# Performance work log

Measured on AMD Instinct MI355X. Metric: run time of the kernel, lower is better.

Reference implementation:

```python
import jax, jax.numpy as jnp
import numpy as np

B, C, N, K, COUT = 8, 128, 10000, 16, 256


def setup_inputs() -> dict:
    key = jax.random.key(0)
    ks = jax.random.split(key, 8)
    x = jax.random.normal(ks[0], (B, C, N, 1), dtype=jnp.float32)
    edge_index = jax.random.randint(ks[1], (2, B, N, K), 0, N)
    s1 = 1.0 / np.sqrt(C)
    W1 = jax.random.uniform(ks[2], (C, C), jnp.float32, -s1, s1)   # nn1 1x1 conv weight
    b1 = jax.random.uniform(ks[3], (C,), jnp.float32, -s1, s1)
    Wp = jax.random.uniform(ks[4], (C, C), jnp.float32, -s1, s1)   # nn_pooling Linear
    bp = jax.random.uniform(ks[5], (C,), jnp.float32, -s1, s1)
    s2 = 1.0 / np.sqrt(2 * C)
    W2 = jax.random.uniform(ks[6], (COUT, 2 * C), jnp.float32, -s2, s2)  # nn2 1x1 conv
    b2 = jax.random.uniform(ks[7], (COUT,), jnp.float32, -s2, s2)
    return dict(x=x, edge_index=edge_index, W1=W1, b1=b1, Wp=Wp, bp=bp, W2=W2, b2=b2)


def reference(x, edge_index, W1, b1, Wp, bp, W2, b2):
    b, c, n, _ = x.shape
    k = edge_index.shape[-1]
    # nn1: 1x1 conv (channel mix) + ReLU -> [B,C,N,1]
    h = jax.nn.relu(jnp.einsum('bcns,dc->bdns', x, W1) + b1[None, :, None, None])
    # batched_index_select: gather neighbor features along vertex dim -> [B,C,N,K]
    hn = h[:, :, :, 0]                              # [B,C,N]
    idx = edge_index[0].reshape(b, 1, n * k)        # broadcast over C
    xj = jnp.take_along_axis(hn, idx, axis=2).reshape(b, c, n, k)
    # nn_pooling: Linear over channel dim + ReLU (transpose(1,3) in torch == act on C)
    xj = jax.nn.relu(jnp.einsum('bcnk,dc->bdnk', xj, Wp) + bp[None, :, None, None])
    # max-pool over neighbors, keepdim -> [B,C,N,1]
    xj = jnp.max(xj, axis=-1, keepdims=True)
    # concat along channels, nn2: 1x1 conv + ReLU -> [B,COUT,N,1]
    cat = jnp.concatenate([h, xj], axis=1)
    out = jax.nn.relu(jnp.einsum('bcns,dc->bdns', cat, W2) + b2[None, :, None, None])
    return out
```

## Files before the change

### kernel.cpp

```cpp
#include <hip/hip_runtime.h>

#define NODES 10000
#define BATCH 8
#define CH    128
#define KNB   16
#define CO    256

typedef __bf16 bf16x8 __attribute__((ext_vector_type(8)));
typedef float  f32x4  __attribute__((ext_vector_type(4)));

__device__ __forceinline__ unsigned short f2bf(float f) {
  unsigned u = __float_as_uint(f);
  u = (u + 0x7FFFu + ((u >> 16) & 1u)) >> 16;
  return (unsigned short)u;
}

__device__ __forceinline__ unsigned pkmax(unsigned a, unsigned b) {
  unsigned d;
  asm("v_pk_max_u16 %0, %1, %2" : "=v"(d) : "v"(a), "v"(b));
  return d;
}
__device__ __forceinline__ uint4 pkmax4(uint4 a, uint4 b) {
  a.x = pkmax(a.x, b.x); a.y = pkmax(a.y, b.y);
  a.z = pkmax(a.z, b.z); a.w = pkmax(a.w, b.w);
  return a;
}
__device__ __forceinline__ bf16x8 asbf8(uint4 u) {
  union { uint4 u; bf16x8 b; } c; c.u = u; return c.b;
}

__global__ __launch_bounds__(256) void prep(
    const float* __restrict__ W1, const float* __restrict__ Wp,
    const float* __restrict__ W2,
    unsigned short* __restrict__ W1b, unsigned short* __restrict__ Wpb,
    unsigned short* __restrict__ W2b)
{
  int i = blockIdx.x * 256 + threadIdx.x;
  const float* src; unsigned short* dst; int off;
  if (i < 4096)      { src = W1; dst = W1b; off = i; }
  else if (i < 8192) { src = Wp; dst = Wpb; off = i - 4096; }
  else               { src = W2; dst = W2b; off = i - 8192; }
  float4 v = ((const float4*)src)[off];
  ushort4 o;
  o.x = f2bf(v.x); o.y = f2bf(v.y); o.z = f2bf(v.z); o.w = f2bf(v.w);
  ((ushort4*)dst)[off] = o;
}

__global__ __launch_bounds__(256) void fused_hz(
    const unsigned short* __restrict__ W1b, const float* __restrict__ b1,
    const unsigned short* __restrict__ Wpb, const float* __restrict__ bp,
    const float* __restrict__ x,
    unsigned short* __restrict__ h_t, unsigned short* __restrict__ z_t)
{
  const int b  = blockIdx.y;
  const int n0 = blockIdx.x * 64;
  const int t  = threadIdx.x;
  const int lane = t & 63, w = t >> 6;
  const int lm = lane & 15, q = lane >> 4;

  __shared__ __align__(16) unsigned short Bt[64 * 128];
  __shared__ __align__(16) unsigned short Ht[64 * 128];
  char* BtB = (char*)Bt;
  char* HtB = (char*)Ht;

  {
    const float* X = x + (size_t)b * CH * NODES;
#pragma unroll
    for (int rep = 0; rep < 4; ++rep) {
      int flat = t + rep * 256;
      int c2 = flat >> 4, n4 = flat & 15;
      int c  = c2 * 2;
      int gn = n0 + n4 * 4;
      float4 a0 = make_float4(0.f,0.f,0.f,0.f), a1 = a0;
      if (gn < NODES) {
        a0 = *(const float4*)(X + (size_t)c * NODES + gn);
        a1 = *(const float4*)(X + (size_t)(c + 1) * NODES + gn);
      }
      float v0[4] = {a0.x, a0.y, a0.z, a0.w};
      float v1[4] = {a1.x, a1.y, a1.z, a1.w};
#pragma unroll
      for (int i = 0; i < 4; ++i) {
        int nn = n4 * 4 + i;
        unsigned pk = (unsigned)f2bf(v0[i]) | ((unsigned)f2bf(v1[i]) << 16);
        int phys = nn * 256 + (((c2 >> 2) ^ (nn & 7)) << 4) + ((c2 & 3) << 2);
        *(unsigned*)(BtB + phys) = pk;
      }
    }
  }

  const int d0  = (w & 1) * 64;
  const int nbw = (w >> 1) * 32;

  uint4 af[4][4];
#pragma unroll
  for (int dt = 0; dt < 4; ++dt)
#pragma unroll
    for (int kt = 0; kt < 4; ++kt)
      af[dt][kt] = *(const uint4*)(W1b + (d0 + dt*16 + lm) * CH + kt*32 + q*8);

  __syncthreads();

  f32x4 acc[4][2];
#pragma unroll
  for (int dt = 0; dt < 4; ++dt)
#pragma unroll
    for (int nt = 0; nt < 2; ++nt) acc[dt][nt] = (f32x4){0.f,0.f,0.f,0.f};

#pragma unroll
  for (int kt = 0; kt < 4; ++kt)
#pragma unroll
    for (int nt = 0; nt < 2; ++nt) {
      int nl = nbw + nt * 16 + lm;
      int chunk = kt * 4 + q;
      int phys = nl * 256 + ((chunk ^ (nl & 7)) << 4);
      bf16x8 bb = asbf8(*(const uint4*)(BtB + phys));
#pragma unroll
      for (int dt = 0; dt < 4; ++dt)
        acc[dt][nt] = __builtin_amdgcn_mfma_f32_16x16x32_bf16(
            asbf8(af[dt][kt]), bb, acc[dt][nt], 0, 0, 0);
    }

  uint4 af2[4][4];
#pragma unroll
  for (int dt = 0; dt < 4; ++dt)
#pragma unroll
    for (int kt = 0; kt < 4; ++kt)
      af2[dt][kt] = *(const uint4*)(Wpb + (d0 + dt*16 + lm) * CH + kt*32 + q*8);

#pragma unroll
  for (int dt = 0; dt < 4; ++dt) {
    int dbase = d0 + dt * 16 + q * 4;
    float4 bi = *(const float4*)(b1 + dbase);
    float bv[4] = {bi.x, bi.y, bi.z, bi.w};
#pragma unroll
    for (int nt = 0; nt < 2; ++nt) {
      int nl = nbw + nt * 16 + lm;
      int gn = n0 + nl;
      ushort4 o;
      o.x = f2bf(fmaxf(acc[dt][nt][0] + bv[0], 0.f));
      o.y = f2bf(fmaxf(acc[dt][nt][1] + bv[1], 0.f));
      o.z = f2bf(fmaxf(acc[dt][nt][2] + bv[2], 0.f));
      o.w = f2bf(fmaxf(acc[dt][nt][3] + bv[3], 0.f));
      int chunk = dbase >> 3;
      int phys  = nl * 256 + ((chunk ^ (nl & 7)) << 4) + ((q & 1) << 3);
      *(ushort4*)(HtB + phys) = o;
      if (gn < NODES)
        *(ushort4*)(h_t + ((size_t)b * NODES + gn) * CH + dbase) = o;
    }
  }

  __syncthreads();

#pragma unroll
  for (int dt = 0; dt < 4; ++dt)
#pragma unroll
    for (int nt = 0; nt < 2; ++nt) acc[dt][nt] = (f32x4){0.f,0.f,0.f,0.f};

#pragma unroll
  for (int kt = 0; kt < 4; ++kt)
#pragma unroll
    for (int nt = 0; nt < 2; ++nt) {
      int nl = nbw + nt * 16 + lm;
      int chunk = kt * 4 + q;
      int phys = nl * 256 + ((chunk ^ (nl & 7)) << 4);
      bf16x8 bb = asbf8(*(const uint4*)(HtB + phys));
#pragma unroll
      for (int dt = 0; dt < 4; ++dt)
        acc[dt][nt] = __builtin_amdgcn_mfma_f32_16x16x32_bf16(
            asbf8(af2[dt][kt]), bb, acc[dt][nt], 0, 0, 0);
    }

#pragma unroll
  for (int dt = 0; dt < 4; ++dt) {
    int dbase = d0 + dt * 16 + q * 4;
    float4 bi = *(const float4*)(bp + dbase);
    float bv[4] = {bi.x, bi.y, bi.z, bi.w};
#pragma unroll
    for (int nt = 0; nt < 2; ++nt) {
      int gn = n0 + nbw + nt * 16 + lm;
      if (gn < NODES) {
        ushort4 o;
        o.x = f2bf(fmaxf(acc[dt][nt][0] + bv[0], 0.f));
        o.y = f2bf(fmaxf(acc[dt][nt][1] + bv[1], 0.f));
        o.z = f2bf(fmaxf(acc[dt][nt][2] + bv[2], 0.f));
        o.w = f2bf(fmaxf(acc[dt][nt][3] + bv[3], 0.f));
        *(ushort4*)(z_t + ((size_t)b * NODES + gn) * CH + dbase) = o;
      }
    }
  }
}

__global__ __launch_bounds__(256) void gmax_kernel(
    const unsigned short* __restrict__ z_t, const int* __restrict__ e0,
    unsigned short* __restrict__ zm)
{
  const int bid = blockIdx.x;
  const int b   = bid & 7;
  const int n0  = (bid >> 3) * 64;
  const int t   = threadIdx.x;
  const int nl  = t >> 2, c = t & 3;
  const int gn  = n0 + nl;
  if (gn >= NODES) return;

  const int* ip = e0 + ((size_t)b * NODES + gn) * KNB;
  int4 iv0 = *(const int4*)(ip);
  int4 iv1 = *(const int4*)(ip + 4);
  int4 iv2 = *(const int4*)(ip + 8);
  int4 iv3 = *(const int4*)(ip + 12);
  int idx[16] = {iv0.x, iv0.y, iv0.z, iv0.w,
                 iv1.x, iv1.y, iv1.z, iv1.w,
                 iv2.x, iv2.y, iv2.z, iv2.w,
                 iv3.x, iv3.y, iv3.z, iv3.w};

  const char* Z = (const char*)(z_t + (size_t)b * NODES * CH) + c * 16;
  uint4 m[4];
#pragma unroll
  for (int cg = 0; cg < 4; ++cg) m[cg] = make_uint4(0u, 0u, 0u, 0u);

#pragma unroll
  for (int k = 0; k < KNB; ++k) {
    const char* p = Z + (size_t)idx[k] * (CH * 2);
#pragma unroll
    for (int cg = 0; cg < 4; ++cg)
      m[cg] = pkmax4(m[cg], *(const uint4*)(p + cg * 64));
  }

  char* O = (char*)(zm + ((size_t)b * NODES + gn) * CH) + c * 16;
#pragma unroll
  for (int cg = 0; cg < 4; ++cg)
    *(uint4*)(O + cg * 64) = m[cg];
}

__global__ __launch_bounds__(256) void out_gemm(
    const unsigned short* __restrict__ h_t, const unsigned short* __restrict__ zm,
    const unsigned short* __restrict__ W2b, const float* __restrict__ b2,
    float* __restrict__ out)
{
  const int bid = blockIdx.x;
  const int b   = bid & 7;
  const int n0  = (bid >> 3) * 64;
  const int t   = threadIdx.x;
  const int lane = t & 63, w = t >> 6;
  const int lm = lane & 15, q = lane >> 4;

  __shared__ __align__(16) unsigned short cat[64 * 256];
  char* catB = (char*)cat;

#pragma unroll
  for (int rep = 0; rep < 8; ++rep) {
    int flat = t + rep * 256;
    int nl = flat >> 5, chunk = flat & 31;
    int gn = n0 + nl;
    uint4 v = make_uint4(0u, 0u, 0u, 0u);
    if (gn < NODES) {
      const unsigned short* src = (chunk < 16)
        ? h_t + ((size_t)b * NODES + gn) * CH + chunk * 8
        : zm  + ((size_t)b * NODES + gn) * CH + (chunk - 16) * 8;
      v = *(const uint4*)src;
    }
    int phys = nl * 512 + ((chunk ^ (nl & 7)) << 4);
    *(uint4*)(catB + phys) = v;
  }
  __syncthreads();

  const int d0 = w * 64;
  f32x4 acc[4][4];
#pragma unroll
  for (int dt = 0; dt < 4; ++dt)
#pragma unroll
    for (int nt = 0; nt < 4; ++nt) acc[dt][nt] = (f32x4){0.f, 0.f, 0.f, 0.f};

  uint4 acur[4], anxt[4];
#pragma unroll
  for (int dt = 0; dt < 4; ++dt)
    acur[dt] = *(const uint4*)(W2b + (d0 + dt * 16 + lm) * CO + q * 8);

#pragma unroll
  for (int kt = 0; kt < 8; ++kt) {
    if (kt < 7) {
#pragma unroll
      for (int dt = 0; dt < 4; ++dt)
        anxt[dt] = *(const uint4*)(W2b + (d0 + dt * 16 + lm) * CO
                                   + (kt + 1) * 32 + q * 8);
    }
#pragma unroll
    for (int nt = 0; nt < 4; ++nt) {
      int nl = nt * 16 + lm;
      int chunk = kt * 4 + q;
      int phys = nl * 512 + ((chunk ^ (nl & 7)) << 4);
      bf16x8 bb = asbf8(*(const uint4*)(catB + phys));
#pragma unroll
      for (int dt = 0; dt < 4; ++dt)
        acc[dt][nt] = __builtin_amdgcn_mfma_f32_16x16x32_bf16(
            asbf8(acur[dt]), bb, acc[dt][nt], 0, 0, 0);
    }
#pragma unroll
    for (int dt = 0; dt < 4; ++dt) acur[dt] = anxt[dt];
  }

#pragma unroll
  for (int dt = 0; dt < 4; ++dt) {
    int dbase = d0 + dt * 16 + q * 4;
    float4 bi = *(const float4*)(b2 + dbase);
    float bv[4] = {bi.x, bi.y, bi.z, bi.w};
#pragma unroll
    for (int nt = 0; nt < 4; ++nt) {
      int gn = n0 + nt * 16 + lm;
      if (gn < NODES) {
        float* op = out + ((size_t)(b * CO + dbase) * NODES) + gn;
#pragma unroll
        for (int r = 0; r < 4; ++r)
          op[(size_t)r * NODES] = fmaxf(acc[dt][nt][r] + bv[r], 0.f);
      }
    }
  }
}

extern "C" void kernel_launch(void* const* d_in, const int* in_sizes, int n_in,
                              void* d_out, int out_size, void* d_ws, size_t ws_size,
                              hipStream_t stream) {
  const float* x  = (const float*)d_in[0];
  const int*   ei = (const int*)d_in[1];
  const float* W1 = (const float*)d_in[2];
  const float* b1 = (const float*)d_in[3];
  const float* Wp = (const float*)d_in[4];
  const float* bp = (const float*)d_in[5];
  const float* W2 = (const float*)d_in[6];
  const float* b2 = (const float*)d_in[7];
  float* out = (float*)d_out;

  unsigned short* ws  = (unsigned short*)d_ws;
  unsigned short* h_t = ws;
  unsigned short* z_t = h_t + (size_t)BATCH * NODES * CH;
  unsigned short* W1b = z_t + (size_t)BATCH * NODES * CH;
  unsigned short* Wpb = W1b + CH * CH;
  unsigned short* W2b = Wpb + CH * CH;
  unsigned short* zm  = W2b + CO * 2 * CH;

  prep<<<96, 256, 0, stream>>>(W1, Wp, W2, W1b, Wpb, W2b);

  const int NT = (NODES + 63) / 64;
  fused_hz<<<dim3(NT, BATCH), 256, 0, stream>>>(W1b, b1, Wpb, bp, x, h_t, z_t);
  gmax_kernel<<<BATCH * NT, 256, 0, stream>>>(z_t, ei, zm);
  out_gemm<<<BATCH * NT, 256, 0, stream>>>(h_t, zm, W2b, b2, out);
}
```

Measured before the change: 207.8 us.

## Process two node tiles per out_gemm block with register-prefetched second tile

Each out_gemm block now handles two consecutive 64-node tiles instead of one. The second tile's h/zm rows are loaded into registers while the first tile's GEMM runs, then written to shared memory after a barrier. This is meant to hide global-load latency behind MFMA compute and to halve the block count. The cost is more registers per thread, two extra barriers, and less grid parallelism.

```diff
diff --git a/kernel.cpp b/kernel.cpp
--- a/kernel.cpp
+++ b/kernel.cpp
@@ -231,38 +231,42 @@
     *(uint4*)(O + cg * 64) = m[cg];
 }
 
-__global__ __launch_bounds__(256) void out_gemm(
-    const unsigned short* __restrict__ h_t, const unsigned short* __restrict__ zm,
-    const unsigned short* __restrict__ W2b, const float* __restrict__ b2,
-    float* __restrict__ out)
-{
-  const int bid = blockIdx.x;
-  const int b   = bid & 7;
-  const int n0  = (bid >> 3) * 64;
-  const int t   = threadIdx.x;
-  const int lane = t & 63, w = t >> 6;
-  const int lm = lane & 15, q = lane >> 4;
-
-  __shared__ __align__(16) unsigned short cat[64 * 256];
-  char* catB = (char*)cat;
-
+__device__ __forceinline__ void og_stage_load(
+    uint4 (&s)[8], const unsigned short* __restrict__ h_t,
+    const unsigned short* __restrict__ zm, size_t nb, int n0, int t)
+{
 #pragma unroll
   for (int rep = 0; rep < 8; ++rep) {
     int flat = t + rep * 256;
     int nl = flat >> 5, chunk = flat & 31;
     int gn = n0 + nl;
-    uint4 v = make_uint4(0u, 0u, 0u, 0u);
+    s[rep] = make_uint4(0u, 0u, 0u, 0u);
     if (gn < NODES) {
       const unsigned short* src = (chunk < 16)
-        ? h_t + ((size_t)b * NODES + gn) * CH + chunk * 8
-        : zm  + ((size_t)b * NODES + gn) * CH + (chunk - 16) * 8;
-      v = *(const uint4*)src;
-    }
+        ? h_t + (nb + gn) * CH + chunk * 8
+        : zm  + (nb + gn) * CH + (chunk - 16) * 8;
+      s[rep] = *(const uint4*)src;
+    }
+  }
+}
+
+__device__ __forceinline__ void og_stage_write(
+    const uint4 (&s)[8], char* catB, int t)
+{
+#pragma unroll
+  for (int rep = 0; rep < 8; ++rep) {
+    int flat = t + rep * 256;
+    int nl = flat >> 5, chunk = flat & 31;
     int phys = nl * 512 + ((chunk ^ (nl & 7)) << 4);
-    *(uint4*)(catB + phys) = v;
-  }
-  __syncthreads();
-
+    *(uint4*)(catB + phys) = s[rep];
+  }
+}
+
+__device__ __forceinline__ void og_compute_tile(
+    const char* catB, const unsigned short* __restrict__ W2b,
+    const float* __restrict__ b2, float* __restrict__ out,
+    int b, int n0, int w, int lm, int q)
+{
   const int d0 = w * 64;
   f32x4 acc[4][4];
 #pragma unroll
@@ -314,6 +318,41 @@
       }
     }
   }
+}
+
+__global__ __launch_bounds__(256) void out_gemm(
+    const unsigned short* __restrict__ h_t, const unsigned short* __restrict__ zm,
+    const unsigned short* __restrict__ W2b, const float* __restrict__ b2,
+    float* __restrict__ out)
+{
+  const int bid = blockIdx.x;
+  const int b   = bid & 7;
+  const int n0A = (bid >> 3) * 128;
+  const int n0B = n0A + 64;
+  const int t   = threadIdx.x;
+  const int lane = t & 63, w = t >> 6;
+  const int lm = lane & 15, q = lane >> 4;
+  const size_t nb = (size_t)b * NODES;
+
+  __shared__ __align__(16) unsigned short cat[64 * 256];
+  char* catB = (char*)cat;
+
+  {
+    uint4 sA[8];
+    og_stage_load(sA, h_t, zm, nb, n0A, t);
+    og_stage_write(sA, catB, t);
+  }
+
+  uint4 sB[8];
+  og_stage_load(sB, h_t, zm, nb, n0B, t);
+
+  __syncthreads();
+  og_compute_tile(catB, W2b, b2, out, b, n0A, w, lm, q);
+  __syncthreads();
+
+  og_stage_write(sB, catB, t);
+  __syncthreads();
+  og_compute_tile(catB, W2b, b2, out, b, n0B, w, lm, q);
 }
 
 extern "C" void kernel_launch(void* const* d_in, const int* in_sizes, int n_in,
@@ -340,7 +379,8 @@
   prep<<<96, 256, 0, stream>>>(W1, Wp, W2, W1b, Wpb, W2b);
 
   const int NT = (NODES + 63) / 64;
+  const int NP = (NT + 1) / 2;
   fused_hz<<<dim3(NT, BATCH), 256, 0, stream>>>(W1b, b1, Wpb, bp, x, h_t, z_t);
   gmax_kernel<<<BATCH * NT, 256, 0, stream>>>(z_t, ei, zm);
-  out_gemm<<<BATCH * NT, 256, 0, stream>>>(h_t, zm, W2b, b2, out);
-}
+  out_gemm<<<BATCH * NP, 256, 0, stream>>>(h_t, zm, W2b, b2, out);
+}
```

After: 221.2 us. +6.4%, slower.

## Pipeline out_gemm with double-buffered LDS and coalesce h/z stores via LDS

Applied to the files above, without the earlier changes.

The output GEMM becomes persistent: 512 blocks each handle two or three node tiles. W2 is held in registers for the whole block, and cat tiles are staged into double-buffered LDS with global_load_lds so the next tile's load overlaps the current tile's MFMAs. fused_hz now writes h and z through LDS and emits full 16-byte row-contiguous stores instead of scattered 8-byte stores. In exchange the kernels carry more registers and LDS, need extra barriers, and launch fewer blocks for out_gemm.

```diff
diff --git a/kernel.cpp b/kernel.cpp
--- a/kernel.cpp
+++ b/kernel.cpp
@@ -27,6 +27,12 @@
 }
 __device__ __forceinline__ bf16x8 asbf8(uint4 u) {
   union { uint4 u; bf16x8 b; } c; c.u = u; return c.b;
+}
+
+__device__ __forceinline__ void gload_lds16(const void* g, void* l) {
+  __builtin_amdgcn_global_load_lds(
+      (const __attribute__((address_space(1))) unsigned int*)g,
+      (__attribute__((address_space(3))) unsigned int*)l, 16, 0, 0);
 }
 
 __global__ __launch_bounds__(256) void prep(
@@ -57,6 +63,7 @@
   const int t  = threadIdx.x;
   const int lane = t & 63, w = t >> 6;
   const int lm = lane & 15, q = lane >> 4;
+  const size_t nb = (size_t)b * NODES;
 
   __shared__ __align__(16) unsigned short Bt[64 * 128];
   __shared__ __align__(16) unsigned short Ht[64 * 128];
@@ -135,7 +142,6 @@
 #pragma unroll
     for (int nt = 0; nt < 2; ++nt) {
       int nl = nbw + nt * 16 + lm;
-      int gn = n0 + nl;
       ushort4 o;
       o.x = f2bf(fmaxf(acc[dt][nt][0] + bv[0], 0.f));
       o.y = f2bf(fmaxf(acc[dt][nt][1] + bv[1], 0.f));
@@ -144,12 +150,23 @@
       int chunk = dbase >> 3;
       int phys  = nl * 256 + ((chunk ^ (nl & 7)) << 4) + ((q & 1) << 3);
       *(ushort4*)(HtB + phys) = o;
+    }
+  }
+
+  __syncthreads();
+
+  {
+    int nl = t >> 2;
+    int gn = n0 + nl;
+#pragma unroll
+    for (int rep = 0; rep < 4; ++rep) {
+      int g = (t & 3) + rep * 4;
+      int phys = nl * 256 + ((g ^ (nl & 7)) << 4);
+      uint4 v = *(const uint4*)(HtB + phys);
       if (gn < NODES)
-        *(ushort4*)(h_t + ((size_t)b * NODES + gn) * CH + dbase) = o;
-    }
-  }
-
-  __syncthreads();
+        *(uint4*)((char*)h_t + (nb + (size_t)gn) * 256 + g * 16) = v;
+    }
+  }
 
 #pragma unroll
   for (int dt = 0; dt < 4; ++dt)
@@ -177,15 +194,30 @@
     float bv[4] = {bi.x, bi.y, bi.z, bi.w};
 #pragma unroll
     for (int nt = 0; nt < 2; ++nt) {
-      int gn = n0 + nbw + nt * 16 + lm;
-      if (gn < NODES) {
-        ushort4 o;
-        o.x = f2bf(fmaxf(acc[dt][nt][0] + bv[0], 0.f));
-        o.y = f2bf(fmaxf(acc[dt][nt][1] + bv[1], 0.f));
-        o.z = f2bf(fmaxf(acc[dt][nt][2] + bv[2], 0.f));
-        o.w = f2bf(fmaxf(acc[dt][nt][3] + bv[3], 0.f));
-        *(ushort4*)(z_t + ((size_t)b * NODES + gn) * CH + dbase) = o;
-      }
+      int nl = nbw + nt * 16 + lm;
+      ushort4 o;
+      o.x = f2bf(fmaxf(acc[dt][nt][0] + bv[0], 0.f));
+      o.y = f2bf(fmaxf(acc[dt][nt][1] + bv[1], 0.f));
+      o.z = f2bf(fmaxf(acc[dt][nt][2] + bv[2], 0.f));
+      o.w = f2bf(fmaxf(acc[dt][nt][3] + bv[3], 0.f));
+      int chunk = dbase >> 3;
+      int phys  = nl * 256 + ((chunk ^ (nl & 7)) << 4) + ((q & 1) << 3);
+      *(ushort4*)(BtB + phys) = o;
+    }
+  }
+
+  __syncthreads();
+
+  {
+    int nl = t >> 2;
+    int gn = n0 + nl;
+#pragma unroll
+    for (int rep = 0; rep < 4; ++rep) {
+      int g = (t & 3) + rep * 4;
+      int phys = nl * 256 + ((g ^ (nl & 7)) << 4);
+      uint4 v = *(const uint4*)(BtB + phys);
+      if (gn < NODES)
+        *(uint4*)((char*)z_t + (nb + (size_t)gn) * 256 + g * 16) = v;
     }
   }
 }
@@ -231,58 +263,35 @@
     *(uint4*)(O + cg * 64) = m[cg];
 }
 
-__global__ __launch_bounds__(256) void out_gemm(
-    const unsigned short* __restrict__ h_t, const unsigned short* __restrict__ zm,
-    const unsigned short* __restrict__ W2b, const float* __restrict__ b2,
-    float* __restrict__ out)
-{
-  const int bid = blockIdx.x;
-  const int b   = bid & 7;
-  const int n0  = (bid >> 3) * 64;
-  const int t   = threadIdx.x;
-  const int lane = t & 63, w = t >> 6;
-  const int lm = lane & 15, q = lane >> 4;
-
-  __shared__ __align__(16) unsigned short cat[64 * 256];
-  char* catB = (char*)cat;
-
+__device__ __forceinline__ void og_stage(
+    unsigned short* buf, const unsigned short* __restrict__ h_t,
+    const unsigned short* __restrict__ zm, size_t nb, int n0, int w, int lane)
+{
 #pragma unroll
   for (int rep = 0; rep < 8; ++rep) {
-    int flat = t + rep * 256;
-    int nl = flat >> 5, chunk = flat & 31;
-    int gn = n0 + nl;
-    uint4 v = make_uint4(0u, 0u, 0u, 0u);
-    if (gn < NODES) {
-      const unsigned short* src = (chunk < 16)
-        ? h_t + ((size_t)b * NODES + gn) * CH + chunk * 8
-        : zm  + ((size_t)b * NODES + gn) * CH + (chunk - 16) * 8;
-      v = *(const uint4*)src;
-    }
-    int phys = nl * 512 + ((chunk ^ (nl & 7)) << 4);
-    *(uint4*)(catB + phys) = v;
-  }
-  __syncthreads();
-
-  const int d0 = w * 64;
-  f32x4 acc[4][4];
+    const int row0 = w * 2 + rep * 8;
+    const int nl = row0 + (lane >> 5);
+    const int l  = (lane & 31) ^ (nl & 7);
+    int gn = n0 + nl; if (gn > NODES - 1) gn = NODES - 1;
+    const unsigned short* src = (l < 16)
+        ? h_t + (nb + (size_t)gn) * CH + l * 8
+        : zm  + (nb + (size_t)gn) * CH + (l - 16) * 8;
+    gload_lds16(src, (char*)buf + row0 * 512);
+  }
+  __builtin_amdgcn_sched_barrier(0);
+}
+
+__device__ __forceinline__ void og_mfma(
+    f32x4 (&acc)[4][4], const unsigned short* buf,
+    const uint4 (&af)[8][4], int lm, int q)
+{
+  const char* catB = (const char*)buf;
 #pragma unroll
   for (int dt = 0; dt < 4; ++dt)
 #pragma unroll
     for (int nt = 0; nt < 4; ++nt) acc[dt][nt] = (f32x4){0.f, 0.f, 0.f, 0.f};
-
-  uint4 acur[4], anxt[4];
-#pragma unroll
-  for (int dt = 0; dt < 4; ++dt)
-    acur[dt] = *(const uint4*)(W2b + (d0 + dt * 16 + lm) * CO + q * 8);
-
-#pragma unroll
-  for (int kt = 0; kt < 8; ++kt) {
-    if (kt < 7) {
-#pragma unroll
-      for (int dt = 0; dt < 4; ++dt)
-        anxt[dt] = *(const uint4*)(W2b + (d0 + dt * 16 + lm) * CO
-                                   + (kt + 1) * 32 + q * 8);
-    }
+#pragma unroll
+  for (int kt = 0; kt < 8; ++kt)
 #pragma unroll
     for (int nt = 0; nt < 4; ++nt) {
       int nl = nt * 16 + lm;
@@ -292,12 +301,15 @@
 #pragma unroll
       for (int dt = 0; dt < 4; ++dt)
         acc[dt][nt] = __builtin_amdgcn_mfma_f32_16x16x32_bf16(
-            asbf8(acur[dt]), bb, acc[dt][nt], 0, 0, 0);
-    }
-#pragma unroll
-    for (int dt = 0; dt < 4; ++dt) acur[dt] = anxt[dt];
-  }
-
+            asbf8(af[kt][dt]), bb, acc[dt][nt], 0, 0, 0);
+    }
+}
+
+__device__ __forceinline__ void og_epi(
+    const f32x4 (&acc)[4][4], const float* __restrict__ b2,
+    float* __restrict__ out, int b, int n0, int w, int lm, int q)
+{
+  const int d0 = w * 64;
 #pragma unroll
   for (int dt = 0; dt < 4; ++dt) {
     int dbase = d0 + dt * 16 + q * 4;
@@ -313,6 +325,64 @@
           op[(size_t)r * NODES] = fmaxf(acc[dt][nt][r] + bv[r], 0.f);
       }
     }
+  }
+}
+
+__global__ __launch_bounds__(256) void out_gemm(
+    const unsigned short* __restrict__ h_t, const unsigned short* __restrict__ zm,
+    const unsigned short* __restrict__ W2b, const float* __restrict__ b2,
+    float* __restrict__ out)
+{
+  const int bid = blockIdx.x;
+  const int b   = bid & 7;
+  const int g   = bid >> 3;
+  const int t   = threadIdx.x;
+  const int lane = t & 63, w = t >> 6;
+  const int lm = lane & 15, q = lane >> 4;
+  const size_t nb = (size_t)b * NODES;
+
+  __shared__ __align__(16) unsigned short bufA[64 * 256];
+  __shared__ __align__(16) unsigned short bufB[64 * 256];
+
+  const int d0 = w * 64;
+  uint4 af[8][4];
+#pragma unroll
+  for (int kt = 0; kt < 8; ++kt)
+#pragma unroll
+    for (int dt = 0; dt < 4; ++dt)
+      af[kt][dt] = *(const uint4*)(W2b + (d0 + dt*16 + lm) * CO + kt*32 + q*8);
+
+  const int n0_0 = g * 64;
+  const int n0_1 = (g + 64) * 64;
+  const int n0_2 = (g + 128) * 64;
+  const bool has2 = (g + 128) < 157;
+
+  f32x4 acc[4][4];
+
+  og_stage(bufA, h_t, zm, nb, n0_0, w, lane);
+  asm volatile("s_waitcnt vmcnt(0)" ::: "memory");
+  __builtin_amdgcn_sched_barrier(0);
+  __builtin_amdgcn_s_barrier();
+
+  og_stage(bufB, h_t, zm, nb, n0_1, w, lane);
+  og_mfma(acc, bufA, af, lm, q);
+  asm volatile("s_waitcnt vmcnt(0)" ::: "memory");
+  __builtin_amdgcn_sched_barrier(0);
+  __builtin_amdgcn_s_barrier();
+  og_epi(acc, b2, out, b, n0_0, w, lm, q);
+
+  if (has2) {
+    og_stage(bufA, h_t, zm, nb, n0_2, w, lane);
+    og_mfma(acc, bufB, af, lm, q);
+    asm volatile("s_waitcnt vmcnt(0)" ::: "memory");
+    __builtin_amdgcn_sched_barrier(0);
+    __builtin_amdgcn_s_barrier();
+    og_epi(acc, b2, out, b, n0_1, w, lm, q);
+    og_mfma(acc, bufA, af, lm, q);
+    og_epi(acc, b2, out, b, n0_2, w, lm, q);
+  } else {
+    og_mfma(acc, bufB, af, lm, q);
+    og_epi(acc, b2, out, b, n0_1, w, lm, q);
   }
 }
 
@@ -342,5 +412,5 @@
   const int NT = (NODES + 63) / 64;
   fused_hz<<<dim3(NT, BATCH), 256, 0, stream>>>(W1b, b1, Wpb, bp, x, h_t, z_t);
   gmax_kernel<<<BATCH * NT, 256, 0, stream>>>(z_t, ei, zm);
-  out_gemm<<<BATCH * NT, 256, 0, stream>>>(h_t, zm, W2b, b2, out);
-}
+  out_gemm<<<512, 256, 0, stream>>>(h_t, zm, W2b, b2, out);
+}
```

New measurement: 199.0 us. 4.3% less time.
